# Optimization experiments

Measured on AMD Instinct MI355X. Metric: run time of the kernel, lower is better.

The kernel has to match this reference:

```python
import jax, jax.numpy as jnp
import numpy as np

SOFTMAX_TEMP = 0.01
CART_PIXEL_WIDTH = 256
CART_RESOLUTION = 0.2592


def zn_desc(desc):
    # desc: B x C x N. Zero-mean, unit-std over channel dim (torch.std default ddof=1).
    mean = jnp.mean(desc, axis=1, keepdims=True)
    std = jnp.std(desc, axis=1, keepdims=True, ddof=1)
    return (desc - mean) / std


def compute_2D_from_3D(coords):
    cart_min_range = (CART_PIXEL_WIDTH / 2 - 0.5) * CART_RESOLUTION
    u = (cart_min_range + coords[:, 1]) / CART_RESOLUTION
    v = (cart_min_range - coords[:, 0]) / CART_RESOLUTION
    return jnp.stack([u, v], axis=2)


def setup_inputs() -> dict:
    key = jax.random.key(0)
    B, C, N, H, W = 2, 256, 1024, 256, 256
    ks = jax.random.split(key, 4)
    tgt_coords = jax.random.normal(ks[0], (B, 3, H * W), jnp.float32) * 10.0
    tgt_weights = jax.random.uniform(ks[1], (B, 1, H, W), dtype=jnp.float32)
    src_desc_norm = zn_desc(jax.random.normal(ks[2], (B, C, N), jnp.float32))
    tgt_desc = jax.random.normal(ks[3], (B, C, H, W), jnp.float32)
    return {
        'geometry_img': jnp.zeros((1,), jnp.int32),
        'tgt_coords': tgt_coords,
        'tgt_2D': jnp.zeros((1,), jnp.int32),
        'tgt_weights': tgt_weights,
        'tgt_weights_dense': jnp.zeros((1,), jnp.int32),
        'src_desc_norm': src_desc_norm,
        'tgt_desc': tgt_desc,
        'tgt_desc_dense': jnp.zeros((1,), jnp.int32),
        'cam_calib': jnp.zeros((1,), jnp.int32),
        'window_size': 16,
    }


def reference(geometry_img, tgt_coords, tgt_2D, tgt_weights, tgt_weights_dense,
              src_desc_norm, tgt_desc, tgt_desc_dense, cam_calib, window_size):
    B, C = tgt_desc.shape[0], tgt_desc.shape[1]
    M = tgt_desc.shape[2] * tgt_desc.shape[3]
    N = src_desc_norm.shape[2]

    tgt_desc_flat = tgt_desc.reshape(B, C, M)
    tgt_desc_norm = zn_desc(tgt_desc_flat)

    # B x N x M similarity (ZNCC): src^T @ tgt / C
    match_vals = jnp.einsum('bcn,bcm->bnm', src_desc_norm, tgt_desc_norm) / float(C)
    soft_match_vals = jax.nn.softmax(match_vals / SOFTMAX_TEMP, axis=2)
    max_softmax = jnp.max(soft_match_vals, axis=(1, 2))  # (B,)

    # three weighted sums sharing the same softmax matrix
    pseudo_coords = jnp.einsum('bcm,bnm->bcn', tgt_coords, soft_match_vals)
    pseudo_weights = jnp.einsum('bcm,bnm->bcn', tgt_weights.reshape(B, 1, M), soft_match_vals)
    pseudo_descs = jnp.einsum('bcm,bnm->bcn', tgt_desc_flat, soft_match_vals)          # B x C x N

    pseudo_2D = compute_2D_from_3D(pseudo_coords)  # B x N x 2
    pseudo_descs = zn_desc(pseudo_descs)
    valid_pts = jnp.ones((B, 1, N), jnp.int32)
    return pseudo_coords, pseudo_weights, pseudo_descs, pseudo_2D, valid_pts, max_softmax
```

## Files before the change

### kernel.cpp

```cpp
#include <hip/hip_runtime.h>
#include <hip/hip_bf16.h>

#define Bb   2
#define Cc   256
#define Nn   1024
#define Mm   65536
#define VROWS 272
#define MSTEP 32

#define SCL_OFF  0L
#define TMC_OFF  524288L
#define TCM_OFF  67633152L
#define SNC_OFF  138936320L
#define PART_OFF 139984896L
#define PS_OFF   PART_OFF
#define PS2_OFF  (PART_OFF + 2097152L)

#define O_COORD 0L
#define O_W     6144L
#define O_DESC  8192L
#define O_P2D   532480L
#define O_VALID 536576L
#define O_MAXSM 538624L

using f32x4 = __attribute__((ext_vector_type(4))) float;
using s16x8 = __attribute__((ext_vector_type(8))) short;

__device__ inline unsigned short f2bf(float x) {
    union { float f; unsigned int u; } v; v.f = x;
    unsigned int r = v.u + 0x7FFFu + ((v.u >> 16) & 1u);
    return (unsigned short)(r >> 16);
}
__device__ inline float bf2f(unsigned short u) {
    union { unsigned int u; float f; } v; v.u = ((unsigned int)u) << 16;
    return v.f;
}
__device__ inline float exp2v(float x) {
    float r; asm("v_exp_f32 %0, %1" : "=v"(r) : "v"(x)); return r;
}
__device__ inline unsigned int cvtpk(float lo, float hi) {
    unsigned int r;
    asm("v_cvt_pk_bf16_f32 %0, %1, %2" : "=v"(r) : "v"(lo), "v"(hi));
    return r;
}

__device__ inline void gld_lds16(const unsigned short* g, unsigned short* l) {
    __builtin_amdgcn_global_load_lds(
        (const __attribute__((address_space(1))) unsigned int*)g,
        (__attribute__((address_space(3))) unsigned int*)l, 16, 0, 0);
}

__global__ void k_prep_tgt(const float* __restrict__ tgt,
                           unsigned short* __restrict__ tmc,
                           unsigned short* __restrict__ tcm,
                           float* __restrict__ ps,
                           float* __restrict__ ps2) {
    __shared__ float lds[64][65];
    __shared__ float sm[4][64], sm2[4][64];
    int b = blockIdx.z, cy = blockIdx.y, c0 = cy * 64;
    long m0 = (long)blockIdx.x * 64;
    int ty = threadIdx.x >> 6, tx = threadIdx.x & 63;
    float s = 0.f, s2 = 0.f;
    #pragma unroll
    for (int k = 0; k < 16; ++k) {
        int ci = 4 * k + ty;
        float v = tgt[((long)b * Cc + c0 + ci) * Mm + m0 + tx];
        lds[ci][tx] = v;
        s += v; s2 += v * v;
        tcm[((long)b * VROWS + c0 + ci) * Mm + m0 + tx] = f2bf(v);
    }
    sm[ty][tx] = s; sm2[ty][tx] = s2;
    __syncthreads();
    #pragma unroll
    for (int k = 0; k < 16; ++k) {
        int mi = 4 * k + ty;
        tmc[((long)b * Mm + m0 + mi) * Cc + c0 + tx] = f2bf(lds[tx][mi]);
    }
    if (ty == 0) {
        long o = ((long)b * 4 + cy) * Mm + m0 + tx;
        ps[o]  = (sm[0][tx] + sm[1][tx]) + (sm[2][tx] + sm[3][tx]);
        ps2[o] = (sm2[0][tx] + sm2[1][tx]) + (sm2[2][tx] + sm2[3][tx]);
    }
}

__global__ void k_stats(const float* __restrict__ ps,
                        const float* __restrict__ ps2,
                        const float* __restrict__ coords,
                        const float* __restrict__ weights,
                        float* __restrict__ scl,
                        unsigned short* __restrict__ tcm) {
    int b = blockIdx.y;
    long m = (long)blockIdx.x * 256 + threadIdx.x;
    float s = 0.f, s2 = 0.f;
    #pragma unroll
    for (int k = 0; k < 4; ++k) {
        long o = ((long)b * 4 + k) * Mm + m;
        s += ps[o]; s2 += ps2[o];
    }
    float var = fmaxf((s2 - s * s * (1.0f / Cc)) * (1.0f / (Cc - 1)), 1e-20f);
    scl[(long)b * Mm + m] = 1.4426950408889634f * rsqrtf(var) * (1.0f / (Cc * 0.01f));
    unsigned short* vrow = tcm + ((long)b * VROWS + 256) * Mm + m;
    #pragma unroll
    for (int i = 0; i < 3; ++i) vrow[(long)i * Mm] = f2bf(coords[((long)b * 3 + i) * Mm + m]);
    vrow[3L * Mm] = f2bf(weights[(long)b * Mm + m]);
    vrow[4L * Mm] = 0x3F80;
    #pragma unroll
    for (int i = 5; i < 16; ++i) vrow[(long)i * Mm] = 0;
}

__global__ void k_prep_src(const float* __restrict__ src, unsigned short* __restrict__ snc) {
    __shared__ float lds[64][65];
    int b = blockIdx.z, c0 = blockIdx.y * 64, n0 = blockIdx.x * 64;
    int ty = threadIdx.x >> 6, tx = threadIdx.x & 63;
    #pragma unroll
    for (int k = 0; k < 16; ++k)
        lds[4 * k + ty][tx] = src[((long)b * Cc + c0 + 4 * k + ty) * Nn + n0 + tx];
    __syncthreads();
    #pragma unroll
    for (int k = 0; k < 16; ++k) {
        int ni = 4 * k + ty;
        snc[((long)b * Nn + n0 + ni) * Cc + c0 + tx] = f2bf(lds[tx][ni]);
    }
}

__global__ __launch_bounds__(256, 2) void k_main(const unsigned short* __restrict__ tmc,
                                                 const unsigned short* __restrict__ tcm,
                                                 const unsigned short* __restrict__ snc,
                                                 const float* __restrict__ scl,
                                                 unsigned short* __restrict__ part,
                                                 float* __restrict__ zp,
                                                 float* __restrict__ pp,
                                                 int mcn) {
    __shared__ __align__(16) unsigned short kb[2][8192];
    __shared__ __align__(16) unsigned short vb[2][8704];
    __shared__ __align__(16) unsigned short pbuf[4][2][16][40];

    int w = threadIdx.x >> 6, lane = threadIdx.x & 63;
    int l15 = lane & 15, lg = lane >> 4;
    int b = blockIdx.z, nt = blockIdx.y, mc = blockIdx.x;
    int nb = nt * 128 + w * 32;
    int mchunk = Mm / mcn;
    int nit = mchunk / MSTEP;
    long mbase = (long)mc * mchunk;

    s16x8 qf[2][8];
    #pragma unroll
    for (int st = 0; st < 2; ++st) {
        const unsigned short* qp = snc + ((long)b * Nn + nb + st * 16 + l15) * Cc + lg * 8;
        #pragma unroll
        for (int cc = 0; cc < 8; ++cc) qf[st][cc] = *(const s16x8*)(qp + cc * 32);
    }

    f32x4 acc[2][17];
    #pragma unroll
    for (int st = 0; st < 2; ++st)
        #pragma unroll
        for (int t = 0; t < 17; ++t) acc[st][t] = (f32x4){0.f, 0.f, 0.f, 0.f};
    float pmax[2] = {0.f, 0.f};

    const unsigned short* tmcb = tmc + (long)b * Mm * Cc;
    const unsigned short* tcmb = tcm + (long)b * VROWS * (long)Mm;
    unsigned koff[4];
    #pragma unroll
    for (int i = 0; i < 4; ++i) {
        int ins = w * 4 + i;
        int row = 2 * ins + (lane >> 5);
        int gs  = (lane & 31) ^ (row & 7);
        koff[i] = (unsigned)((mbase + row) * Cc + gs * 8);
    }
    unsigned voff[5];
    int vj = ((lane & 3) ^ ((lane >> 3) & 3)) * 8;
    #pragma unroll
    for (int i = 0; i < 5; ++i) {
        int ins = (i < 4) ? (w * 4 + i) : 16;
        int row = ins * 16 + (lane >> 2);
        voff[i] = (unsigned)((long)row * Mm + mbase + vj);
    }

    const float* sclb = scl + (long)b * Mm;

    auto stage = [&](int d) {
        unsigned short* kd = kb[d];
        unsigned short* vd = vb[d];
        #pragma unroll
        for (int i = 0; i < 4; ++i) gld_lds16(tmcb + koff[i], kd + (w * 4 + i) * 512);
        #pragma unroll
        for (int i = 0; i < 4; ++i) gld_lds16(tcmb + voff[i], vd + (w * 4 + i) * 512);
        if (w == 3) gld_lds16(tcmb + voff[4], vd + 16 * 512);
        #pragma unroll
        for (int i = 0; i < 4; ++i) koff[i] += MSTEP * Cc;
        #pragma unroll
        for (int i = 0; i < 5; ++i) voff[i] += MSTEP;
    };

    int ksw = (l15 & 7) << 3;
    int vsw = (lg ^ ((l15 >> 1) & 3)) * 8;

    stage(0);
    __syncthreads();

    for (int s = 0; s < nit; ++s) {
        int cur = s & 1;
        if (s + 1 < nit) stage(cur ^ 1);
        const unsigned short* kbc = kb[cur];
        const unsigned short* vbc = vb[cur];
        long m0 = mbase + (long)s * MSTEP;
        float4 sc0 = *(const float4*)(sclb + m0 + lg * 4);
        float4 sc1 = *(const float4*)(sclb + m0 + 16 + lg * 4);

        #pragma unroll
        for (int t = 0; t < 2; ++t) {
            f32x4 dA = (f32x4){0.f, 0.f, 0.f, 0.f};
            f32x4 dB = (f32x4){0.f, 0.f, 0.f, 0.f};
            const unsigned short* kr = kbc + (t * 16 + l15) * Cc;
            #pragma unroll
            for (int cc = 0; cc < 8; ++cc) {
                s16x8 kf = *(const s16x8*)(kr + ((cc * 32 + lg * 8) ^ ksw));
                dA = __builtin_amdgcn_mfma_f32_16x16x32_bf16(kf, qf[0][cc], dA, 0, 0, 0);
                dB = __builtin_amdgcn_mfma_f32_16x16x32_bf16(kf, qf[1][cc], dB, 0, 0, 0);
            }
            float4 sc = t ? sc1 : sc0;
            #pragma unroll
            for (int st = 0; st < 2; ++st) {
                f32x4 d = st ? dB : dA;
                float p0 = exp2v(d.x * sc.x);
                float p1 = exp2v(d.y * sc.y);
                float p2 = exp2v(d.z * sc.z);
                float p3 = exp2v(d.w * sc.w);
                pmax[st] = fmaxf(pmax[st], fmaxf(fmaxf(p0, p1), fmaxf(p2, p3)));
                unsigned long long pk =
                    (unsigned long long)cvtpk(p0, p1) | ((unsigned long long)cvtpk(p2, p3) << 32);
                *(unsigned long long*)&pbuf[w][st][l15][t * 16 + lg * 4] = pk;
            }
        }
        s16x8 pfA = *(const s16x8*)&pbuf[w][0][l15][lg * 8];
        s16x8 pfB = *(const s16x8*)&pbuf[w][1][l15][lg * 8];
        #pragma unroll
        for (int t = 0; t < 17; ++t) {
            s16x8 vf = *(const s16x8*)(vbc + (t * 16 + l15) * MSTEP + vsw);
            acc[0][t] = __builtin_amdgcn_mfma_f32_16x16x32_bf16(vf, pfA, acc[0][t], 0, 0, 0);
            acc[1][t] = __builtin_amdgcn_mfma_f32_16x16x32_bf16(vf, pfB, acc[1][t], 0, 0, 0);
        }
        __syncthreads();
    }

    #pragma unroll
    for (int st = 0; st < 2; ++st) {
        float pt = fmaxf(pmax[st], __shfl_xor(pmax[st], 16));
        pt = fmaxf(pt, __shfl_xor(pt, 32));
        long zi = ((long)(b * mcn + mc)) * Nn + nb + st * 16;
        if (lg == 1) zp[zi + l15] = acc[st][16].x;
        if (lane < 16) pp[zi + lane] = pt;
        unsigned short* po = part + (((long)(b * mcn + mc) * Nn) + nb + st * 16 + l15) * VROWS;
        #pragma unroll
        for (int t = 0; t < 17; ++t) {
            f32x4 a = acc[st][t];
            unsigned long long pk =
                (unsigned long long)cvtpk(a.x, a.y) | ((unsigned long long)cvtpk(a.z, a.w) << 32);
            *(unsigned long long*)&po[t * 16 + lg * 4] = pk;
        }
    }
}

__global__ void k_epi(const unsigned short* __restrict__ part,
                      const float* __restrict__ zp,
                      const float* __restrict__ pp,
                      float* __restrict__ out,
                      int mcn) {
    int w = threadIdx.x >> 6, lane = threadIdx.x & 63;
    int bn = blockIdx.x * 4 + w;
    int b = bn >> 10, n = bn & 1023;

    float Z = 0.f, pm = 0.f;
    for (int mc = 0; mc < mcn; ++mc) {
        long zi = ((long)(b * mcn + mc)) * Nn + n;
        Z += zp[zi];
        pm = fmaxf(pm, pp[zi]);
    }
    float invZ = 1.0f / Z;

    float dv[4], s1 = 0.f, s2 = 0.f;
    #pragma unroll
    for (int k = 0; k < 4; ++k) {
        int c = lane + 64 * k;
        float s = 0.f;
        for (int mc = 0; mc < mcn; ++mc)
            s += bf2f(part[((long)(b * mcn + mc) * Nn + n) * VROWS + c]);
        float d = s * invZ;
        dv[k] = d; s1 += d; s2 += d * d;
    }
    #pragma unroll
    for (int off = 1; off < 64; off <<= 1) { s1 += __shfl_xor(s1, off); s2 += __shfl_xor(s2, off); }
    float mean = s1 * (1.0f / 256.0f);
    float var = fmaxf((s2 - 256.0f * mean * mean) * (1.0f / 255.0f), 1e-20f);
    float istd = 1.0f / sqrtf(var);
    #pragma unroll
    for (int k = 0; k < 4; ++k)
        out[O_DESC + ((long)b * Cc + lane + 64 * k) * Nn + n] = (dv[k] - mean) * istd;

    float ex = 0.f;
    if (lane < 4) {
        int c = 256 + lane;
        for (int mc = 0; mc < mcn; ++mc)
            ex += bf2f(part[((long)(b * mcn + mc) * Nn + n) * VROWS + c]);
        ex *= invZ;
    }
    float pc0 = __shfl(ex, 0), pc1 = __shfl(ex, 1), pc2 = __shfl(ex, 2), wv = __shfl(ex, 3);
    if (lane == 0) {
        out[O_COORD + ((long)b * 3 + 0) * Nn + n] = pc0;
        out[O_COORD + ((long)b * 3 + 1) * Nn + n] = pc1;
        out[O_COORD + ((long)b * 3 + 2) * Nn + n] = pc2;
        out[O_W + (long)b * Nn + n] = wv;
        const float cmin = 33.048f;
        out[O_P2D + ((long)b * Nn + n) * 2 + 0] = (cmin + pc1) * (1.0f / 0.2592f);
        out[O_P2D + ((long)b * Nn + n) * 2 + 1] = (cmin - pc0) * (1.0f / 0.2592f);
        out[O_VALID + (long)b * Nn + n] = 1.0f;
        atomicMax((unsigned int*)out + O_MAXSM + b, __float_as_uint(pm * invZ));
    }
}

extern "C" void kernel_launch(void* const* d_in, const int* in_sizes, int n_in,
                              void* d_out, int out_size, void* d_ws, size_t ws_size,
                              hipStream_t stream) {
    const float* tgt_coords  = (const float*)d_in[1];
    const float* tgt_weights = (const float*)d_in[3];
    const float* src_desc    = (const float*)d_in[5];
    const float* tgt_desc    = (const float*)d_in[6];

    char* ws = (char*)d_ws;
    float* scl           = (float*)(ws + SCL_OFF);
    unsigned short* tmc  = (unsigned short*)(ws + TMC_OFF);
    unsigned short* tcm  = (unsigned short*)(ws + TCM_OFF);
    unsigned short* snc  = (unsigned short*)(ws + SNC_OFF);
    unsigned short* part = (unsigned short*)(ws + PART_OFF);
    float* ps            = (float*)(ws + PS_OFF);
    float* ps2           = (float*)(ws + PS2_OFF);
    float* out           = (float*)d_out;

    long need32 = PART_OFF + (long)Bb * 32 * Nn * VROWS * 2 + 2L * Bb * 32 * Nn * 4;
    int mcn = (ws_size >= (size_t)need32) ? 32 : 16;
    long zp_off = PART_OFF + (long)Bb * mcn * Nn * VROWS * 2;
    long pp_off = zp_off + (long)Bb * mcn * Nn * 4;
    float* zp = (float*)(ws + zp_off);
    float* pp = (float*)(ws + pp_off);

    k_prep_tgt<<<dim3(Mm / 64, Cc / 64, Bb), 256, 0, stream>>>(tgt_desc, tmc, tcm, ps, ps2);
    k_stats<<<dim3(Mm / 256, Bb), 256, 0, stream>>>(ps, ps2, tgt_coords, tgt_weights, scl, tcm);
    k_prep_src<<<dim3(Nn / 64, Cc / 64, Bb), 256, 0, stream>>>(src_desc, snc);
    k_main<<<dim3(mcn, Nn / 128, Bb), 256, 0, stream>>>(tmc, tcm, snc, scl, part, zp, pp, mcn);
    (void)hipMemsetAsync((char*)d_out + O_MAXSM * 4, 0, 2 * sizeof(float), stream);
    k_epi<<<dim3((Bb * Nn) / 4), 256, 0, stream>>>(part, zp, pp, out, mcn);
}
```

Baseline: 285.9 us.

## Permute K tile row order so softmax probabilities feed the PV MFMA from registers

Permutes the order in which target rows are loaded into the K LDS tile so that the QK MFMA output layout matches the B-operand layout of the following PV MFMA. The exponentiated probabilities can then be packed directly into registers instead of going through a per-wave LDS buffer (pbuf). The scale-vector loads are reindexed to match the new row mapping. This removes LDS writes and reads plus the LDS footprint of pbuf, but relies on the row permutation being consistent with the V tile column order.

After: 279.2 us. 2.3% less time.

```diff
diff --git a/kernel.cpp b/kernel.cpp
--- a/kernel.cpp
+++ b/kernel.cpp
@@ -133,7 +133,6 @@
                                                  int mcn) {
     __shared__ __align__(16) unsigned short kb[2][8192];
     __shared__ __align__(16) unsigned short vb[2][8704];
-    __shared__ __align__(16) unsigned short pbuf[4][2][16][40];
 
     int w = threadIdx.x >> 6, lane = threadIdx.x & 63;
     int l15 = lane & 15, lg = lane >> 4;
@@ -164,9 +163,10 @@
     #pragma unroll
     for (int i = 0; i < 4; ++i) {
         int ins = w * 4 + i;
-        int row = 2 * ins + (lane >> 5);
-        int gs  = (lane & 31) ^ (row & 7);
-        koff[i] = (unsigned)((mbase + row) * Cc + gs * 8);
+        int a   = 2 * ins + (lane >> 5);
+        int pa  = ((a >> 2) & 3) * 8 + ((a >> 4) << 2) + (a & 3);
+        int gs  = (lane & 31) ^ (a & 7);
+        koff[i] = (unsigned)((mbase + pa) * Cc + gs * 8);
     }
     unsigned voff[5];
     int vj = ((lane & 3) ^ ((lane >> 3) & 3)) * 8;
@@ -205,9 +205,10 @@
         const unsigned short* kbc = kb[cur];
         const unsigned short* vbc = vb[cur];
         long m0 = mbase + (long)s * MSTEP;
-        float4 sc0 = *(const float4*)(sclb + m0 + lg * 4);
-        float4 sc1 = *(const float4*)(sclb + m0 + 16 + lg * 4);
-
+        float4 sc0 = *(const float4*)(sclb + m0 + lg * 8);
+        float4 sc1 = *(const float4*)(sclb + m0 + lg * 8 + 4);
+
+        unsigned int pwA[4], pwB[4];
         #pragma unroll
         for (int t = 0; t < 2; ++t) {
             f32x4 dA = (f32x4){0.f, 0.f, 0.f, 0.f};
@@ -220,21 +221,32 @@
                 dB = __builtin_amdgcn_mfma_f32_16x16x32_bf16(kf, qf[1][cc], dB, 0, 0, 0);
             }
             float4 sc = t ? sc1 : sc0;
-            #pragma unroll
-            for (int st = 0; st < 2; ++st) {
-                f32x4 d = st ? dB : dA;
-                float p0 = exp2v(d.x * sc.x);
-                float p1 = exp2v(d.y * sc.y);
-                float p2 = exp2v(d.z * sc.z);
-                float p3 = exp2v(d.w * sc.w);
-                pmax[st] = fmaxf(pmax[st], fmaxf(fmaxf(p0, p1), fmaxf(p2, p3)));
-                unsigned long long pk =
-                    (unsigned long long)cvtpk(p0, p1) | ((unsigned long long)cvtpk(p2, p3) << 32);
-                *(unsigned long long*)&pbuf[w][st][l15][t * 16 + lg * 4] = pk;
+            {
+                float p0 = exp2v(dA.x * sc.x);
+                float p1 = exp2v(dA.y * sc.y);
+                float p2 = exp2v(dA.z * sc.z);
+                float p3 = exp2v(dA.w * sc.w);
+                pmax[0] = fmaxf(pmax[0], fmaxf(fmaxf(p0, p1), fmaxf(p2, p3)));
+                pwA[t * 2 + 0] = cvtpk(p0, p1);
+                pwA[t * 2 + 1] = cvtpk(p2, p3);
+            }
+            {
+                float p0 = exp2v(dB.x * sc.x);
+                float p1 = exp2v(dB.y * sc.y);
+                float p2 = exp2v(dB.z * sc.z);
+                float p3 = exp2v(dB.w * sc.w);
+                pmax[1] = fmaxf(pmax[1], fmaxf(fmaxf(p0, p1), fmaxf(p2, p3)));
+                pwB[t * 2 + 0] = cvtpk(p0, p1);
+                pwB[t * 2 + 1] = cvtpk(p2, p3);
             }
         }
-        s16x8 pfA = *(const s16x8*)&pbuf[w][0][l15][lg * 8];
-        s16x8 pfB = *(const s16x8*)&pbuf[w][1][l15][lg * 8];
+        union PU { unsigned int u[4]; s16x8 f; };
+        PU puA, puB;
+        #pragma unroll
+        for (int j = 0; j < 4; ++j) { puA.u[j] = pwA[j]; puB.u[j] = pwB[j]; }
+        s16x8 pfA = puA.f;
+        s16x8 pfB = puB.f;
+
         #pragma unroll
         for (int t = 0; t < 17; ++t) {
             s16x8 vf = *(const s16x8*)(vbc + (t * 16 + l15) * MSTEP + vsw);
```
